# Optimization experiments

Measured on AMD Instinct MI355X. Metric: run time of the kernel, lower is better.

## Reference

```python
import jax, jax.numpy as jnp
import numpy as np

N, E, R, C_IN, C_OUT = 100000, 1600000, 6, 8, 16
EPS = 1e-8


def setup_inputs() -> dict:
    key = jax.random.key(0)
    ks = jax.random.split(key, 6)
    x = jax.random.normal(ks[0], (N, C_IN), dtype=jnp.float32)
    supp_edges = jax.random.randint(ks[1], (E, 2), 0, N, dtype=jnp.int64)
    # (E, R, 2): real/imag of precomputed complex stencil (radial bins x transport x weights)
    lift_sten = jax.random.normal(ks[2], (E, R, 2), dtype=jnp.float32) * 0.1
    # TransField learned radial weights (real) and per-channel phase offsets (ftype=1)
    weight = jax.random.normal(ks[3], (R, C_IN, C_OUT), dtype=jnp.float32) * np.float32(1.0 / np.sqrt(R * C_IN))
    offset = jax.random.normal(ks[4], (C_IN, C_OUT), dtype=jnp.float32)
    # TangentNonLin per-channel magnitude bias (modReLU)
    bias = jax.random.normal(ks[5], (C_OUT,), dtype=jnp.float32) * 0.1
    return {"x": x, "supp_edges": supp_edges, "lift_sten": lift_sten,
            "weight": weight, "offset": offset, "bias": bias}


def reference(x, supp_edges, lift_sten, weight, offset, bias):
    src = supp_edges[:, 0]  # j: source
    dst = supp_edges[:, 1]  # i: target
    sten = jax.lax.complex(lift_sten[..., 0], lift_sten[..., 1])          # (E, R) complex64
    xj = x[src]                                                           # (E, Cin) gather
    # per-edge complex message over radial bins and input channels
    msg = sten[:, :, None] * xj[:, None, :].astype(sten.dtype)            # (E, R, Cin)
    agg = jax.ops.segment_sum(msg, dst, num_segments=N)                   # (N, R, Cin)
    # learned filter: real radial weights with per-channel phase offsets exp(i*theta)
    phase = jax.lax.complex(jnp.cos(offset), jnp.sin(offset))             # (Cin, Cout)
    filt = weight.astype(phase.dtype) * phase[None, :, :]                 # (R, Cin, Cout)
    y = jnp.einsum('nrc,rco->no', agg, filt)                              # (N, Cout) complex
    # TangentNonLin: modReLU on magnitude, phase preserved
    mag = jnp.abs(y)
    scale = jax.nn.relu(mag + bias[None, :]) / (mag + EPS)
    y = y * scale.astype(y.dtype)
    # return real/imag stacked for a real-valued output tensor (N, Cout, 2)
    return jnp.stack([jnp.real(y), jnp.imag(y)], axis=-1)
```

## Files before the change

### kernel.cpp

```cpp
#include <hip/hip_runtime.h>
#include <hip/hip_fp16.h>
#include <math.h>

#define N_NODES 100000
#define N_EDGES 1600000
#define RR      6
#define CIN     8
#define COUT    16
#define EPS     1e-8f

#define NBLK_A  512
#define ABLOCK  1024
#define CHUNK   (N_EDGES / NBLK_A)

#define NKEY    782
#define QCAP3   2304

#define LDS_SPAY   0
#define LDS_SHDR   75000
#define LDS_SBKT   87500
#define LDS_CNT    93752
#define LDS_TOTAL  106368

#define BLDS_SPAY  0
#define BLDS_IDXS  55296
#define BLDS_FRE   64512
#define BLDS_FIM   67584
#define BLDS_CNT   70656
#define BLDS_NBASE 71168
#define BLDS_CUR2  71680
#define BLDS_BSH   72192
#define BLDS_TOTAL 72320

__device__ inline unsigned int pack_f16(float a, float b) {
    __half2 h = __floats2half2_rn(a, b);
    return *(unsigned int*)&h;
}

__global__ __launch_bounds__(ABLOCK)
void partition_kernel(const int* __restrict__ edges,
                      const float* __restrict__ sten,
                      int* __restrict__ gcur,
                      unsigned int* __restrict__ hdr,
                      unsigned int* __restrict__ pay) {
    extern __shared__ char smem[];
    uint2*          spay = (uint2*)(smem + LDS_SPAY);
    unsigned int*   shdr = (unsigned int*)(smem + LDS_SHDR);
    unsigned short* sbkt = (unsigned short*)(smem + LDS_SBKT);
    int* cnt   = (int*)(smem + LDS_CNT);
    int* cur   = cnt + NKEY;
    int* base  = cur + NKEY;
    int* gbase = base + NKEY;

    int tid = threadIdx.x;
    int blk = blockIdx.x;
    int e0 = blk * CHUNK;

    for (int i = tid; i < NKEY; i += ABLOCK) { cnt[i] = 0; cur[i] = 0; }
    __syncthreads();

    for (int i = tid; i < CHUNK; i += ABLOCK) {
        int2 ed = ((const int2*)edges)[e0 + i];
        atomicAdd(&cnt[ed.y >> 7], 1);
    }
    __syncthreads();

    if (tid < 64) {
        int lane = tid;
        int off = 0;
        for (int c = 0; c < NKEY; c += 64) {
            int idx = c + lane;
            int v = (idx < NKEY) ? cnt[idx] : 0;
            int orig = v;
#pragma unroll
            for (int d = 1; d < 64; d <<= 1) {
                int t = __shfl_up(v, d);
                if (lane >= d) v += t;
            }
            if (idx < NKEY) base[idx] = off + v - orig;
            off += __shfl(v, 63);
        }
    }
    __syncthreads();

    for (int b = tid; b < NKEY; b += ABLOCK) {
        int c = cnt[b];
        gbase[b] = (c > 0) ? atomicAdd(&gcur[b], c) : 0;
    }
    __syncthreads();

    for (int i = tid; i < CHUNK; i += ABLOCK) {
        int e = e0 + i;
        int2 ed = ((const int2*)edges)[e];
        int b = ed.y >> 7;
        int p = base[b] + atomicAdd(&cur[b], 1);
        sbkt[p] = (unsigned short)b;
        shdr[p] = ((unsigned int)ed.x << 8) | (unsigned int)(ed.y & 255);
        const float4* sp = (const float4*)(sten + (size_t)e * 12);
        float4 s0 = sp[0], s1 = sp[1], s2 = sp[2];
        uint2* dp = spay + p * 3;
        dp[0] = (uint2){ pack_f16(s0.x, s0.y), pack_f16(s0.z, s0.w) };
        dp[1] = (uint2){ pack_f16(s1.x, s1.y), pack_f16(s1.z, s1.w) };
        dp[2] = (uint2){ pack_f16(s2.x, s2.y), pack_f16(s2.z, s2.w) };
    }
    __syncthreads();

    for (int p = tid; p < CHUNK; p += ABLOCK) {
        int b = (int)sbkt[p];
        int rel = p - base[b];
        long long slot = (long long)gbase[b] + rel;
        if (slot < QCAP3) {
            size_t rs = (size_t)b * QCAP3 + slot;
            hdr[rs] = shdr[p];
            const uint2* sp = spay + p * 3;
            uint2 w0 = sp[0], w1 = sp[1], w2 = sp[2];
            unsigned int* dp = pay + rs * 6;
            *(uint2*)(dp + 0) = w0;
            *(uint2*)(dp + 2) = w1;
            *(uint2*)(dp + 4) = w2;
        }
    }
}

__global__ __launch_bounds__(512, 4)
void bucket_kernel(const float* __restrict__ x,
                   const float* __restrict__ weight,
                   const float* __restrict__ offset,
                   const float* __restrict__ bias,
                   const int* __restrict__ gcur,
                   const unsigned int* __restrict__ hdr,
                   const unsigned int* __restrict__ pay,
                   float* __restrict__ out) {
    extern __shared__ char smem[];
    uint2*        spay  = (uint2*)(smem + BLDS_SPAY);
    unsigned int* idxs  = (unsigned int*)(smem + BLDS_IDXS);
    float*        fre   = (float*)(smem + BLDS_FRE);
    float*        fim   = (float*)(smem + BLDS_FIM);
    int*          cnt   = (int*)(smem + BLDS_CNT);
    int*          nbase = (int*)(smem + BLDS_NBASE);
    int*          cur2  = (int*)(smem + BLDS_CUR2);
    float*        bsh   = (float*)(smem + BLDS_BSH);

    int tid = threadIdx.x;
    int key = blockIdx.x;

    for (int i = tid; i < RR * CIN * COUT; i += 512) {
        int co = i % (CIN * COUT);
        float w = weight[i], off = offset[co];
        fre[i] = w * cosf(off);
        fim[i] = w * sinf(off);
    }
    if (tid < COUT) bsh[tid] = bias[tid];
    if (tid < 128) { cnt[tid] = 0; cur2[tid] = 0; }

    int T = gcur[key];
    if (T > QCAP3) T = QCAP3;

    const unsigned int* hslice = hdr + (size_t)key * QCAP3;

    {
        const uint2* psrc = (const uint2*)(pay + (size_t)key * QCAP3 * 6);
        int tw = T * 3;
        for (int i = tid; i < tw; i += 512) spay[i] = psrc[i];
    }

    for (int j = tid; j < T; j += 512) {
        unsigned int h = hslice[j];
        atomicAdd(&cnt[h & 127u], 1);
    }
    __syncthreads();

    if (tid < 128) {
        int lane = tid & 63;
        int half = tid >> 6;
        int v = cnt[tid];
        int orig = v;
#pragma unroll
        for (int d = 1; d < 64; d <<= 1) {
            int t = __shfl_up(v, d);
            if (lane >= d) v += t;
        }
        nbase[tid] = v - orig;
        if (lane == 63 && half == 0) cur2[127] = v;
    }
    __syncthreads();
    if (tid >= 64 && tid < 128) nbase[tid] += cur2[127];
    if (tid == 127) cur2[127] = 0;
    __syncthreads();

    for (int j = tid; j < T; j += 512) {
        unsigned int h = hslice[j];
        int d = (int)(h & 127u);
        int pos = nbase[d] + atomicAdd(&cur2[d], 1);
        idxs[pos] = ((h >> 8) << 12) | (unsigned int)j;
    }
    __syncthreads();

    int local = tid >> 2;
    int n = key * 128 + local;
    int l = tid & 3;
    if (n >= N_NODES) return;

    int deg  = cnt[local];
    int base = nbase[local];

    float ar[RR][2] = {};
    float ai[RR][2] = {};

    uint2 p0 = {}, p1 = {}, p2 = {};
    float2 xv = {};
    if (deg > 0) {
        unsigned int pk = idxs[base];
        int j   = (int)(pk & 4095u);
        int src = (int)(pk >> 12);
        const uint2* pp = spay + j * 3;
        p0 = pp[0]; p1 = pp[1]; p2 = pp[2];
        xv = *(const float2*)(x + (size_t)src * CIN + 2 * l);
    }
    for (int k = 0; k < deg; ++k) {
        uint2 q0 = {}, q1 = {}, q2 = {};
        float2 nx = {};
        if (k + 1 < deg) {
            unsigned int pk = idxs[base + k + 1];
            int j   = (int)(pk & 4095u);
            int src = (int)(pk >> 12);
            const uint2* pp = spay + j * 3;
            q0 = pp[0]; q1 = pp[1]; q2 = pp[2];
            nx = *(const float2*)(x + (size_t)src * CIN + 2 * l);
        }
        unsigned int wv[6] = {p0.x, p0.y, p1.x, p1.y, p2.x, p2.y};
#pragma unroll
        for (int r = 0; r < RR; ++r) {
            __half2 hh = *(__half2*)&wv[r];
            float sre = __half2float(__low2half(hh));
            float sim = __half2float(__high2half(hh));
            ar[r][0] = fmaf(sre, xv.x, ar[r][0]);
            ar[r][1] = fmaf(sre, xv.y, ar[r][1]);
            ai[r][0] = fmaf(sim, xv.x, ai[r][0]);
            ai[r][1] = fmaf(sim, xv.y, ai[r][1]);
        }
        p0 = q0; p1 = q1; p2 = q2; xv = nx;
    }

    float yr[COUT], yi[COUT];
#pragma unroll
    for (int o = 0; o < COUT; ++o) { yr[o] = 0.f; yi[o] = 0.f; }
#pragma unroll
    for (int r = 0; r < RR; ++r) {
#pragma unroll
        for (int j = 0; j < 2; ++j) {
            int c = 2 * l + j;
            float are = ar[r][j], aim = ai[r][j];
            const float* fr = &fre[(r * CIN + c) * COUT];
            const float* fi = &fim[(r * CIN + c) * COUT];
#pragma unroll
            for (int o = 0; o < COUT; ++o) {
                yr[o] = fmaf(are, fr[o], yr[o]);
                yr[o] = fmaf(-aim, fi[o], yr[o]);
                yi[o] = fmaf(are, fi[o], yi[o]);
                yi[o] = fmaf(aim, fr[o], yi[o]);
            }
        }
    }
#pragma unroll
    for (int o = 0; o < COUT; ++o) {
        yr[o] += __shfl_xor(yr[o], 1);
        yr[o] += __shfl_xor(yr[o], 2);
        yi[o] += __shfl_xor(yi[o], 1);
        yi[o] += __shfl_xor(yi[o], 2);
    }
    float tmp[8];
    int ob = 4 * l;
#pragma unroll
    for (int j = 0; j < 4; ++j) {
        int o = ob + j;
        float re = yr[o], im = yi[o];
        float mag = sqrtf(re * re + im * im);
        float sc = fmaxf(mag + bsh[o], 0.f) / (mag + EPS);
        tmp[2 * j]     = re * sc;
        tmp[2 * j + 1] = im * sc;
    }
    float4* op = (float4*)(out + (size_t)n * 2 * COUT + 8 * l);
    op[0] = ((const float4*)tmp)[0];
    op[1] = ((const float4*)tmp)[1];
}

extern "C" void kernel_launch(void* const* d_in, const int* in_sizes, int n_in,
                              void* d_out, int out_size, void* d_ws, size_t ws_size,
                              hipStream_t stream) {
    const float* x      = (const float*)d_in[0];
    const int*   edges  = (const int*)d_in[1];
    const float* sten   = (const float*)d_in[2];
    const float* weight = (const float*)d_in[3];
    const float* offset = (const float*)d_in[4];
    const float* bias   = (const float*)d_in[5];
    float* out = (float*)d_out;

    int* gcur = (int*)d_ws;
    unsigned int* hdr = (unsigned int*)((char*)d_ws + 8192);
    unsigned int* pay = hdr + (size_t)NKEY * QCAP3;

    static int lds_inited = 0;
    if (!lds_inited) {
        (void)hipFuncSetAttribute((const void*)partition_kernel,
                                  hipFuncAttributeMaxDynamicSharedMemorySize,
                                  LDS_TOTAL);
        (void)hipFuncSetAttribute((const void*)bucket_kernel,
                                  hipFuncAttributeMaxDynamicSharedMemorySize,
                                  BLDS_TOTAL);
        lds_inited = 1;
    }

    (void)hipMemsetAsync(gcur, 0, sizeof(int) * NKEY, stream);

    partition_kernel<<<NBLK_A, ABLOCK, LDS_TOTAL, stream>>>(edges, sten, gcur, hdr, pay);
    bucket_kernel<<<NKEY, 512, BLDS_TOTAL, stream>>>(x, weight, offset, bias,
                                                     gcur, hdr, pay, out);
}
```

Baseline: 239.2 us.

## Scatter payloads into node-sorted padded LDS and sort nodes by degree

The bucket kernel stops bulk-copying the edge payloads into LDS and then reading them through an index indirection. Each thread now scatters its payload and source id straight into a destination-sorted, padded LDS layout, which removes the idxs array and the extra index lookup per edge. The padding is meant to reduce LDS bank conflicts. A 128-element bitonic sort by degree then assigns nodes to waves so that lanes in a wave have similar loop trip counts, at the cost of several extra barriers and scattered global reads during the scatter pass.

```diff
diff --git a/kernel.cpp b/kernel.cpp
--- a/kernel.cpp
+++ b/kernel.cpp
@@ -23,19 +23,23 @@
 #define LDS_TOTAL  106368
 
 #define BLDS_SPAY  0
-#define BLDS_IDXS  55296
-#define BLDS_FRE   64512
-#define BLDS_FIM   67584
-#define BLDS_CNT   70656
-#define BLDS_NBASE 71168
-#define BLDS_CUR2  71680
-#define BLDS_BSH   72192
-#define BLDS_TOTAL 72320
+#define BLDS_SSRC  56448
+#define BLDS_FRE   66240
+#define BLDS_FIM   69312
+#define BLDS_CNT   72384
+#define BLDS_NBASE 72896
+#define BLDS_CUR2  73408
+#define BLDS_BSH   73920
+#define BLDS_PERM  73984
+#define BLDS_TOTAL 74496
 
 __device__ inline unsigned int pack_f16(float a, float b) {
     __half2 h = __floats2half2_rn(a, b);
     return *(unsigned int*)&h;
 }
+
+__device__ inline int payA(int pos) { return pos * 24 + ((pos >> 4) << 3); }
+__device__ inline int srcS(int pos) { return (pos + (pos >> 4)) << 2; }
 
 __global__ __launch_bounds__(ABLOCK)
 void partition_kernel(const int* __restrict__ edges,
@@ -132,14 +136,13 @@
                    const unsigned int* __restrict__ pay,
                    float* __restrict__ out) {
     extern __shared__ char smem[];
-    uint2*        spay  = (uint2*)(smem + BLDS_SPAY);
-    unsigned int* idxs  = (unsigned int*)(smem + BLDS_IDXS);
     float*        fre   = (float*)(smem + BLDS_FRE);
     float*        fim   = (float*)(smem + BLDS_FIM);
     int*          cnt   = (int*)(smem + BLDS_CNT);
     int*          nbase = (int*)(smem + BLDS_NBASE);
     int*          cur2  = (int*)(smem + BLDS_CUR2);
     float*        bsh   = (float*)(smem + BLDS_BSH);
+    unsigned int* perm  = (unsigned int*)(smem + BLDS_PERM);
 
     int tid = threadIdx.x;
     int key = blockIdx.x;
@@ -152,17 +155,13 @@
     }
     if (tid < COUT) bsh[tid] = bias[tid];
     if (tid < 128) { cnt[tid] = 0; cur2[tid] = 0; }
+    __syncthreads();
 
     int T = gcur[key];
     if (T > QCAP3) T = QCAP3;
 
     const unsigned int* hslice = hdr + (size_t)key * QCAP3;
-
-    {
-        const uint2* psrc = (const uint2*)(pay + (size_t)key * QCAP3 * 6);
-        int tw = T * 3;
-        for (int i = tid; i < tw; i += 512) spay[i] = psrc[i];
-    }
+    const uint2* psrc = (const uint2*)(pay + (size_t)key * QCAP3 * 6);
 
     for (int j = tid; j < T; j += 512) {
         unsigned int h = hslice[j];
@@ -192,17 +191,39 @@
         unsigned int h = hslice[j];
         int d = (int)(h & 127u);
         int pos = nbase[d] + atomicAdd(&cur2[d], 1);
-        idxs[pos] = ((h >> 8) << 12) | (unsigned int)j;
-    }
-    __syncthreads();
-
-    int local = tid >> 2;
+        *(unsigned int*)(smem + BLDS_SSRC + srcS(pos)) = h >> 8;
+        const uint2* pp = psrc + j * 3;
+        uint2 w0 = pp[0], w1 = pp[1], w2 = pp[2];
+        char* dst = smem + BLDS_SPAY + payA(pos);
+        *(uint2*)(dst + 0)  = w0;
+        *(uint2*)(dst + 8)  = w1;
+        *(uint2*)(dst + 16) = w2;
+    }
+
+    if (tid < 128) perm[tid] = ((unsigned int)cnt[tid] << 8) | (unsigned int)tid;
+    __syncthreads();
+    for (int k2 = 2; k2 <= 128; k2 <<= 1) {
+        for (int jj = k2 >> 1; jj > 0; jj >>= 1) {
+            if (tid < 128) {
+                int ixj = tid ^ jj;
+                if (ixj > tid) {
+                    unsigned int a = perm[tid], c = perm[ixj];
+                    bool up = ((tid & k2) == 0);
+                    if (up ? (a > c) : (a < c)) { perm[tid] = c; perm[ixj] = a; }
+                }
+            }
+            __syncthreads();
+        }
+    }
+
+    int rank = tid >> 2;
+    int l = tid & 3;
+    unsigned int pk = perm[rank];
+    int local = (int)(pk & 127u);
+    int deg   = (int)(pk >> 8);
+    int base  = nbase[local];
     int n = key * 128 + local;
-    int l = tid & 3;
     if (n >= N_NODES) return;
-
-    int deg  = cnt[local];
-    int base = nbase[local];
 
     float ar[RR][2] = {};
     float ai[RR][2] = {};
@@ -210,22 +231,24 @@
     uint2 p0 = {}, p1 = {}, p2 = {};
     float2 xv = {};
     if (deg > 0) {
-        unsigned int pk = idxs[base];
-        int j   = (int)(pk & 4095u);
-        int src = (int)(pk >> 12);
-        const uint2* pp = spay + j * 3;
-        p0 = pp[0]; p1 = pp[1]; p2 = pp[2];
+        int pos = base;
+        const char* pp = smem + BLDS_SPAY + payA(pos);
+        p0 = *(const uint2*)(pp + 0);
+        p1 = *(const uint2*)(pp + 8);
+        p2 = *(const uint2*)(pp + 16);
+        int src = (int)*(const unsigned int*)(smem + BLDS_SSRC + srcS(pos));
         xv = *(const float2*)(x + (size_t)src * CIN + 2 * l);
     }
     for (int k = 0; k < deg; ++k) {
         uint2 q0 = {}, q1 = {}, q2 = {};
         float2 nx = {};
         if (k + 1 < deg) {
-            unsigned int pk = idxs[base + k + 1];
-            int j   = (int)(pk & 4095u);
-            int src = (int)(pk >> 12);
-            const uint2* pp = spay + j * 3;
-            q0 = pp[0]; q1 = pp[1]; q2 = pp[2];
+            int pos = base + k + 1;
+            const char* pp = smem + BLDS_SPAY + payA(pos);
+            q0 = *(const uint2*)(pp + 0);
+            q1 = *(const uint2*)(pp + 8);
+            q2 = *(const uint2*)(pp + 16);
+            int src = (int)*(const unsigned int*)(smem + BLDS_SSRC + srcS(pos));
             nx = *(const float2*)(x + (size_t)src * CIN + 2 * l);
         }
         unsigned int wv[6] = {p0.x, p0.y, p1.x, p1.y, p2.x, p2.y};
```

Result: no change. 238.8 us (-0.2%).

## Read edge payload from global via L2 prefetch, sort nodes by degree in bucket kernel

Applied to the files above, without the earlier changes.

The bucket kernel no longer stages each bucket's payload into LDS. A dummy read loop touches the payload so it sits in cache, and the per-edge loop then reads it straight from global memory. LDS use drops from about 72 KB to about 18 KB of static shared memory. A 128-entry bitonic sort by degree assigns nodes to thread groups so wavefronts get similar loop lengths, and the launch bound is relaxed to 2 blocks per CU. The costs are global and L2 latency on every payload read in place of LDS hits, the chance that the empty asm loop is optimized poorly, and extra barriers for the sort.

```diff
diff --git a/kernel.cpp b/kernel.cpp
--- a/kernel.cpp
+++ b/kernel.cpp
@@ -21,16 +21,6 @@
 #define LDS_SBKT   87500
 #define LDS_CNT    93752
 #define LDS_TOTAL  106368
-
-#define BLDS_SPAY  0
-#define BLDS_IDXS  55296
-#define BLDS_FRE   64512
-#define BLDS_FIM   67584
-#define BLDS_CNT   70656
-#define BLDS_NBASE 71168
-#define BLDS_CUR2  71680
-#define BLDS_BSH   72192
-#define BLDS_TOTAL 72320
 
 __device__ inline unsigned int pack_f16(float a, float b) {
     __half2 h = __floats2half2_rn(a, b);
@@ -122,7 +112,7 @@
     }
 }
 
-__global__ __launch_bounds__(512, 4)
+__global__ __launch_bounds__(512, 2)
 void bucket_kernel(const float* __restrict__ x,
                    const float* __restrict__ weight,
                    const float* __restrict__ offset,
@@ -131,15 +121,12 @@
                    const unsigned int* __restrict__ hdr,
                    const unsigned int* __restrict__ pay,
                    float* __restrict__ out) {
-    extern __shared__ char smem[];
-    uint2*        spay  = (uint2*)(smem + BLDS_SPAY);
-    unsigned int* idxs  = (unsigned int*)(smem + BLDS_IDXS);
-    float*        fre   = (float*)(smem + BLDS_FRE);
-    float*        fim   = (float*)(smem + BLDS_FIM);
-    int*          cnt   = (int*)(smem + BLDS_CNT);
-    int*          nbase = (int*)(smem + BLDS_NBASE);
-    int*          cur2  = (int*)(smem + BLDS_CUR2);
-    float*        bsh   = (float*)(smem + BLDS_BSH);
+    __shared__ unsigned int idxs[QCAP3];
+    __shared__ float fre[RR * CIN * COUT];
+    __shared__ float fim[RR * CIN * COUT];
+    __shared__ int cnt[128], nbase[128], cur2[128];
+    __shared__ float bsh[COUT];
+    __shared__ unsigned int perm[128];
 
     int tid = threadIdx.x;
     int key = blockIdx.x;
@@ -152,16 +139,17 @@
     }
     if (tid < COUT) bsh[tid] = bias[tid];
     if (tid < 128) { cnt[tid] = 0; cur2[tid] = 0; }
+    __syncthreads();
 
     int T = gcur[key];
     if (T > QCAP3) T = QCAP3;
 
     const unsigned int* hslice = hdr + (size_t)key * QCAP3;
-
-    {
-        const uint2* psrc = (const uint2*)(pay + (size_t)key * QCAP3 * 6);
-        int tw = T * 3;
-        for (int i = tid; i < tw; i += 512) spay[i] = psrc[i];
+    const uint2* psrc = (const uint2*)(pay + (size_t)key * QCAP3 * 6);
+
+    for (int i = tid; i < T * 3; i += 512) {
+        uint2 v = psrc[i];
+        asm volatile("" :: "v"(v.x), "v"(v.y));
     }
 
     for (int j = tid; j < T; j += 512) {
@@ -194,15 +182,31 @@
         int pos = nbase[d] + atomicAdd(&cur2[d], 1);
         idxs[pos] = ((h >> 8) << 12) | (unsigned int)j;
     }
-    __syncthreads();
-
-    int local = tid >> 2;
+
+    if (tid < 128) perm[tid] = ((unsigned int)cnt[tid] << 8) | (unsigned int)tid;
+    __syncthreads();
+    for (int k2 = 2; k2 <= 128; k2 <<= 1) {
+        for (int jj = k2 >> 1; jj > 0; jj >>= 1) {
+            if (tid < 128) {
+                int ixj = tid ^ jj;
+                if (ixj > tid) {
+                    unsigned int a = perm[tid], c = perm[ixj];
+                    bool up = ((tid & k2) == 0);
+                    if (up ? (a > c) : (a < c)) { perm[tid] = c; perm[ixj] = a; }
+                }
+            }
+            __syncthreads();
+        }
+    }
+
+    int rank = tid >> 2;
+    int l = tid & 3;
+    unsigned int pk0 = perm[rank];
+    int local = (int)(pk0 & 127u);
+    int deg   = (int)(pk0 >> 8);
+    int base  = nbase[local];
     int n = key * 128 + local;
-    int l = tid & 3;
     if (n >= N_NODES) return;
-
-    int deg  = cnt[local];
-    int base = nbase[local];
 
     float ar[RR][2] = {};
     float ai[RR][2] = {};
@@ -213,7 +217,7 @@
         unsigned int pk = idxs[base];
         int j   = (int)(pk & 4095u);
         int src = (int)(pk >> 12);
-        const uint2* pp = spay + j * 3;
+        const uint2* pp = psrc + j * 3;
         p0 = pp[0]; p1 = pp[1]; p2 = pp[2];
         xv = *(const float2*)(x + (size_t)src * CIN + 2 * l);
     }
@@ -224,7 +228,7 @@
             unsigned int pk = idxs[base + k + 1];
             int j   = (int)(pk & 4095u);
             int src = (int)(pk >> 12);
-            const uint2* pp = spay + j * 3;
+            const uint2* pp = psrc + j * 3;
             q0 = pp[0]; q1 = pp[1]; q2 = pp[2];
             nx = *(const float2*)(x + (size_t)src * CIN + 2 * l);
         }
@@ -305,15 +309,12 @@
         (void)hipFuncSetAttribute((const void*)partition_kernel,
                                   hipFuncAttributeMaxDynamicSharedMemorySize,
                                   LDS_TOTAL);
-        (void)hipFuncSetAttribute((const void*)bucket_kernel,
-                                  hipFuncAttributeMaxDynamicSharedMemorySize,
-                                  BLDS_TOTAL);
         lds_inited = 1;
     }
 
     (void)hipMemsetAsync(gcur, 0, sizeof(int) * NKEY, stream);
 
     partition_kernel<<<NBLK_A, ABLOCK, LDS_TOTAL, stream>>>(edges, sten, gcur, hdr, pay);
-    bucket_kernel<<<NKEY, 512, BLDS_TOTAL, stream>>>(x, weight, offset, bias,
-                                                     gcur, hdr, pay, out);
+    bucket_kernel<<<NKEY, 512, 0, stream>>>(x, weight, offset, bias,
+                                            gcur, hdr, pay, out);
 }
```

After: 218.9 us. 8.5% less time.
